# Kernel optimization log

Hardware: AMD Instinct MI355X
Metric: run time of the kernel (lower is better)

Reference implementation:

```python
import jax, jax.numpy as jnp
import numpy as np

N, E, B, M = 50000, 100000, 50, 50
NPG = N // B            # atoms per graph
DIN, H1, H2, DE, AAF, G = 32, 32, 64, 16, 95, 128
K, T = 3, 6             # ARMA num_stacks, num_layers
F1, F2, F3 = 64, 32, 16
EA = 2 * (M - 1)        # amino-acid edges per graph


def setup_inputs() -> dict:
    key = jax.random.key(0)
    ks = jax.random.split(key, 24)
    s = 0.05
    def w(k, shape):
        return jax.random.normal(k, shape, jnp.float32) * s
    return {
        "x": jax.random.normal(ks[0], (N, DIN), jnp.float32),
        "edge_attr": jax.random.normal(ks[1], (E, DE), jnp.float32),
        "aa_features": jax.random.normal(ks[2], (B, M, AAF), jnp.float32),
        "edge_index": jax.random.randint(ks[3], (2, E), 0, N),
        "monomer_labels": jax.random.randint(ks[4], (B, NPG), 0, M),
        "amino_edge_index": jax.random.randint(ks[5], (2, EA), 0, M),
        "W_e1": w(ks[6], (DE, DIN * H1)), "b_e1": jnp.zeros((DIN * H1,), jnp.float32),
        "root1": w(ks[7], (DIN, H1)), "bias1": jnp.zeros((H1,), jnp.float32),
        "W_e2": w(ks[8], (DE, H1 * H2)), "b_e2": jnp.zeros((H1 * H2,), jnp.float32),
        "root2": w(ks[9], (H1, H2)), "bias2": jnp.zeros((H2,), jnp.float32),
        "Wa_atom": w(ks[10], (H2, 1)), "ba_atom": jnp.zeros((1,), jnp.float32),
        "arma_init_w": w(ks[11], (K, H2 + AAF, G)),
        "arma_w": w(ks[12], (T - 1, K, G, G)),
        "arma_root_w": w(ks[13], (T, K, H2 + AAF, G)),
        "arma_bias": jnp.zeros((T, K, G), jnp.float32),
        "Wa_aa": w(ks[14], (G, 1)), "ba_aa": jnp.zeros((1,), jnp.float32),
        "W1": w(ks[15], (G, F1)), "b1": jnp.zeros((F1,), jnp.float32),
        "W2": w(ks[16], (F1, F2)), "b2": jnp.zeros((F2,), jnp.float32),
        "W3": w(ks[17], (F2, F3)), "b3": jnp.zeros((F3,), jnp.float32),
        "W4": w(ks[18], (F3, 1)), "b4": jnp.zeros((1,), jnp.float32),
    }


def _nnconv(h, src, dst, edge_attr, Wm, bm, root, bias, fin, fout):
    # NNConv (aggr='add'): edge MLP -> per-edge weight matrix, gather-matmul-scatter
    w_e = (edge_attr @ Wm + bm).reshape(-1, fin, fout)            # [E, fin, fout]
    msg = jnp.einsum('ef,efo->eo', h[src], w_e)                   # [E, fout]
    agg = jax.ops.segment_sum(msg, dst, num_segments=h.shape[0])  # scatter-add to targets
    return agg + h @ root + bias


def _forward(x, edge_attr, aa_features, W_e1, b_e1, root1, bias1, W_e2, b_e2, root2, bias2,
             Wa_atom, ba_atom, arma_init_w, arma_w, arma_root_w, arma_bias, Wa_aa, ba_aa,
             W1, b1, W2, b2, W3, b3, W4, b4, edge_index, monomer_labels, amino_edge_index):
    src, dst = edge_index[0], edge_index[1]
    h = jax.nn.relu(_nnconv(x, src, dst, edge_attr, W_e1, b_e1, root1, bias1, DIN, H1))
    h = jax.nn.relu(_nnconv(h, src, dst, edge_attr, W_e2, b_e2, root2, bias2, H1, H2))

    # per-graph attention readout over atoms -> amino-acid embeddings (scatter by monomer label)
    xg = h.reshape(B, NPG, H2)
    attn = jax.nn.softmax(xg @ Wa_atom + ba_atom, axis=1)         # softmax over atoms in graph
    wx = xg * attn
    aa = jax.vmap(lambda wxi, lbl: jax.ops.segment_sum(wxi, lbl, num_segments=M))(wx, monomer_labels)
    h_aa = jnp.concatenate([aa, aa_features], axis=-1)            # [B, M, H2+95]

    # ARMAConv: gcn_norm without self-loops on amino-acid graph (shared across graphs)
    asrc, adst = amino_edge_index[0], amino_edge_index[1]
    deg = jax.ops.segment_sum(jnp.ones((EA,), x.dtype), adst, num_segments=M)
    dinv = jnp.where(deg > 0, 1.0 / jnp.sqrt(jnp.maximum(deg, 1.0)), 0.0)
    norm = dinv[asrc] * dinv[adst]                                # [EA]

    def arma(x0):  # x0: [M, H2+95]
        out = jnp.einsum('mf,kfo->kmo', x0, arma_init_w)          # [K, M, G]
        for t in range(T):
            if t > 0:
                out = jnp.einsum('kmo,kop->kmp', out, arma_w[t - 1])
            msg = out[:, asrc] * norm[None, :, None]              # [K, EA, G]
            prop = jax.vmap(lambda m: jax.ops.segment_sum(m, adst, num_segments=M))(msg)
            rootc = jnp.einsum('mf,kfo->kmo', x0, arma_root_w[t])
            out = jax.nn.relu(prop + rootc + arma_bias[t][:, None, :])
        return out.mean(axis=0)                                   # mean over stacks -> [M, G]

    g = jax.vmap(arma)(h_aa)                                      # [B, M, G]

    # attention readout over amino acids
    attn2 = jax.nn.softmax(g @ Wa_aa + ba_aa, axis=1)
    p = jnp.sum(g * attn2, axis=1)                                # [B, G]

    p = jax.nn.relu(p @ W1 + b1)
    p = jax.nn.relu(p @ W2 + b2)
    p = jax.nn.relu(p @ W3 + b3)
    p = p @ W4 + b4
    return p.reshape(-1)                                          # [B]


def reference(x, edge_attr, aa_features, edge_index, monomer_labels, amino_edge_index,
              W_e1, b_e1, root1, bias1, W_e2, b_e2, root2, bias2, Wa_atom, ba_atom,
              arma_init_w, arma_w, arma_root_w, arma_bias, Wa_aa, ba_aa,
              W1, b1, W2, b2, W3, b3, W4, b4):
    return _forward(x, edge_attr, aa_features, W_e1, b_e1, root1, bias1, W_e2, b_e2, root2, bias2,
                    Wa_atom, ba_atom, arma_init_w, arma_w, arma_root_w, arma_bias, Wa_aa, ba_aa,
                    W1, b1, W2, b2, W3, b3, W4, b4, edge_index, monomer_labels, amino_edge_index)
```

## Files before the change

### kernel.cpp

```cpp
#include <hip/hip_runtime.h>
#include <math.h>

#define N_ATOMS 50000
#define E_EDGES 100000
#define B_G     50
#define M_M     50
#define NPG     1000
#define DIN     32
#define H1C     32
#define H2C     64
#define DEC     16
#define AAF     95
#define G_DIM   128
#define K_ST    3
#define T_L     6
#define EA_E    98
#define XDIM    159
#define NS      21
#define MPAD    64
#define GP      132
#define GPS     136
#define KP2     168
#define KW      544
#define SLC     10
#define APB     100
#define NSB     ((N_ATOMS + 255) / 256)

#define OFF_WE2 (H1C * KW)
#define OFF_WT  (OFF_WE2 + H2C * KW)
#define OFF_AW  (OFF_WT + NS * XDIM * G_DIM)
#define OFF_DEG (OFF_AW + (T_L - 1) * K_ST * G_DIM * G_DIM)
#define PREP_TOTAL (OFF_DEG + E_EDGES)

typedef __attribute__((ext_vector_type(8))) short bf16x8;
typedef __attribute__((ext_vector_type(4))) float f32x4;
typedef __attribute__((ext_vector_type(4))) unsigned int u32x4;

__device__ __forceinline__ short f2bf(float f) {
    unsigned int u = __float_as_uint(f);
    unsigned int r = (u + 0x7FFFu + ((u >> 16) & 1u)) >> 16;
    return (short)r;
}
__device__ __forceinline__ float bf2f(short b) {
    return __uint_as_float(((unsigned int)(unsigned short)b) << 16);
}
__device__ __forceinline__ unsigned int cvtpk_bf16(float lo, float hi) {
    unsigned int r;
    asm("v_cvt_pk_bf16_f32 %0, %1, %2" : "=v"(r) : "v"(lo), "v"(hi));
    return r;
}

__device__ __forceinline__ void f4fma(float4& d, float s, const float4& v) {
    d.x += s * v.x; d.y += s * v.y; d.z += s * v.z; d.w += s * v.w;
}
__device__ __forceinline__ void f4add(float4& d, const float4& v) {
    d.x += v.x; d.y += v.y; d.z += v.z; d.w += v.w;
}
__device__ __forceinline__ void f4relu(float4& d) {
    d.x = fmaxf(d.x, 0.f); d.y = fmaxf(d.y, 0.f);
    d.z = fmaxf(d.z, 0.f); d.w = fmaxf(d.w, 0.f);
}

__global__ __launch_bounds__(256) void prep_all(
    const float* __restrict__ We1, const float* __restrict__ be1, short* __restrict__ WB1,
    const float* __restrict__ We2, const float* __restrict__ be2, short* __restrict__ WB2,
    const float* __restrict__ init_w, const float* __restrict__ root_w, short* __restrict__ Wtb,
    const float* __restrict__ arma_w, short* __restrict__ Wab,
    const int* __restrict__ eidx, int* __restrict__ deg,
    const int* __restrict__ aei, int* __restrict__ aa_off,
    int* __restrict__ aa_src, float* __restrict__ aa_nrm)
{
    int tid = threadIdx.x;
    if (blockIdx.x == 0) {
        __shared__ int   sdeg[M_M];
        __shared__ int   scur[M_M];
        __shared__ float sdinv[M_M];
        __shared__ int   soff[M_M + 1];
        if (tid < M_M) { sdeg[tid] = 0; scur[tid] = 0; }
        __syncthreads();
        if (tid < EA_E) atomicAdd(&sdeg[aei[EA_E + tid]], 1);
        __syncthreads();
        if (tid < M_M) {
            float dv = (float)sdeg[tid];
            sdinv[tid] = (dv > 0.f) ? (1.f / sqrtf(fmaxf(dv, 1.f))) : 0.f;
        }
        __syncthreads();
        if (tid == 0) {
            soff[0] = 0;
            for (int m = 0; m < M_M; ++m) soff[m + 1] = soff[m] + sdeg[m];
        }
        __syncthreads();
        if (tid < EA_E) {
            int ss = aei[tid], dd = aei[EA_E + tid];
            int pos = atomicAdd(&scur[dd], 1);
            int idx = soff[dd] + pos;
            aa_src[idx] = ss;
            aa_nrm[idx] = sdinv[ss] * sdinv[dd];
        }
        if (tid < M_M + 1) aa_off[tid] = soff[tid];
        return;
    }
    int idx = (blockIdx.x - 1) * 256 + tid;
    if (idx < OFF_WE2) {
        int o = idx / KW, k = idx - o * KW;
        float v = (k < 512) ? We1[(size_t)k * H1C + o]
                            : be1[(size_t)(k - 512) * H1C + o];
        WB1[idx] = f2bf(v);
    } else if (idx < OFF_WT) {
        int rem = idx - OFF_WE2;
        int o = rem / KW, k = rem - o * KW;
        float v = (k < 512) ? We2[(size_t)k * H2C + o]
                            : be2[(size_t)(k - 512) * H2C + o];
        WB2[rem] = f2bf(v);
    } else if (idx < OFF_AW) {
        int rem = idx - OFF_WT;
        int s = rem / (XDIM * G_DIM);
        int r2 = rem - s * XDIM * G_DIM;
        int k = r2 / G_DIM, n = r2 - k * G_DIM;
        float v = (s < K_ST) ? init_w[rem]
                             : root_w[(size_t)(s - K_ST) * XDIM * G_DIM + r2];
        Wtb[(size_t)s * G_DIM * KP2 + n * KP2 + k] = f2bf(v);
    } else if (idx < OFF_DEG) {
        int rem = idx - OFF_AW;
        int slot = rem / (G_DIM * G_DIM);
        int r2 = rem - slot * G_DIM * G_DIM;
        int p = r2 / G_DIM, n = r2 - p * G_DIM;
        Wab[(size_t)slot * G_DIM * G_DIM + n * G_DIM + p] = f2bf(arma_w[rem]);
    } else if (idx < PREP_TOTAL) {
        int e = idx - OFF_DEG;
        atomicAdd(&deg[eidx[E_EDGES + e]], 1);
    }
}

__global__ __launch_bounds__(256) void scan_part(const int* __restrict__ deg,
                                                 int* __restrict__ bsum)
{
    __shared__ int tmp[256];
    int tid = threadIdx.x;
    int n = blockIdx.x * 256 + tid;
    tmp[tid] = (n < N_ATOMS) ? deg[n] : 0;
    __syncthreads();
    for (int off = 128; off > 0; off >>= 1) {
        if (tid < off) tmp[tid] += tmp[tid + off];
        __syncthreads();
    }
    if (tid == 0) bsum[blockIdx.x] = tmp[0];
}

__global__ __launch_bounds__(256) void scan_mid(const int* __restrict__ bsum,
                                                int* __restrict__ bpre)
{
    __shared__ int tmp[256];
    int tid = threadIdx.x;
    int v = (tid < NSB) ? bsum[tid] : 0;
    tmp[tid] = v;
    __syncthreads();
    for (int off = 1; off < 256; off <<= 1) {
        int t = tmp[tid];
        int add = (tid >= off) ? tmp[tid - off] : 0;
        __syncthreads();
        tmp[tid] = t + add;
        __syncthreads();
    }
    if (tid < NSB) bpre[tid] = tmp[tid] - v;
}

__global__ __launch_bounds__(256) void scan_out(int* __restrict__ deg_off,
                                                const int* __restrict__ bpre)
{
    __shared__ int tmp[256];
    int tid = threadIdx.x;
    int n = blockIdx.x * 256 + tid;
    int v = (n < N_ATOMS) ? deg_off[n] : 0;
    tmp[tid] = v;
    __syncthreads();
    for (int off = 1; off < 256; off <<= 1) {
        int t = tmp[tid];
        int add = (tid >= off) ? tmp[tid - off] : 0;
        __syncthreads();
        tmp[tid] = t + add;
        __syncthreads();
    }
    int incl = tmp[tid];
    int base = bpre[blockIdx.x];
    if (n < N_ATOMS) deg_off[n] = base + incl - v;
    if (n == N_ATOMS - 1) deg_off[N_ATOMS] = base + incl;
}

template<int FOUT, int NTT, int WGRP, int MTB, bool CIPOS>
__global__ __launch_bounds__(256) void edge_msg_v2(
    const float* __restrict__ h, const float* __restrict__ ea,
    const int* __restrict__ eidx, int* __restrict__ ipos,
    const int* __restrict__ off, int* __restrict__ cursor,
    const short* __restrict__ WB, float* __restrict__ msg)
{
    constexpr int KS = 17;
    __shared__ int iplds[MTB * 16];
    int tid  = threadIdx.x;
    int lane = tid & 63, wave = tid >> 6;
    int l16  = lane & 15, quad = lane >> 4;
    int nt   = wave % NTT, tg = wave / NTT;
    int ebase = blockIdx.x * (MTB * 16);

    if (CIPOS) {
        if (tid < MTB * 16) {
            int e = ebase + tid;
            if (e < E_EDGES) {
                int d = eidx[E_EDGES + e];
                int pos = atomicAdd(&cursor[d], 1);
                int p = off[d] + pos;
                iplds[tid] = p;
                ipos[e] = p;
            }
        }
    }

    bf16x8 Bfr[KS];
    {
        const short* wb = WB + (size_t)(nt * 16 + l16) * KW;
        #pragma unroll
        for (int ks = 0; ks < KS; ++ks)
            Bfr[ks] = *(const bf16x8*)(wb + ks * 32 + quad * 8);
    }
    if (CIPOS) __syncthreads();

    for (int t = tg; t < MTB; t += WGRP) {
        int e  = ebase + t * 16 + l16;
        int es = (e < E_EDGES) ? e : (E_EDGES - 1);
        int s  = eidx[es];
        float4 h0 = *(const float4*)(h + (size_t)s * 32 + quad * 8);
        float4 h1 = *(const float4*)(h + (size_t)s * 32 + quad * 8 + 4);
        float hf[8] = {h0.x, h0.y, h0.z, h0.w, h1.x, h1.y, h1.z, h1.w};
        float4 e0 = *(const float4*)(ea + (size_t)es * DEC);
        float4 e1 = *(const float4*)(ea + (size_t)es * DEC + 4);
        float4 e2 = *(const float4*)(ea + (size_t)es * DEC + 8);
        float4 e3 = *(const float4*)(ea + (size_t)es * DEC + 12);
        float eaf[16] = {e0.x, e0.y, e0.z, e0.w, e1.x, e1.y, e1.z, e1.w,
                         e2.x, e2.y, e2.z, e2.w, e3.x, e3.y, e3.z, e3.w};

        f32x4 acc = (f32x4){0.f, 0.f, 0.f, 0.f};
        #pragma unroll
        for (int ks = 0; ks < KS; ++ks) {
            u32x4 av;
            if (ks < DEC) {
                float fac = eaf[ks];
                #pragma unroll
                for (int j = 0; j < 4; ++j)
                    av[j] = cvtpk_bf16(fac * hf[2 * j], fac * hf[2 * j + 1]);
            } else {
                #pragma unroll
                for (int j = 0; j < 4; ++j)
                    av[j] = cvtpk_bf16(hf[2 * j], hf[2 * j + 1]);
            }
            bf16x8 a = __builtin_bit_cast(bf16x8, av);
            acc = __builtin_amdgcn_mfma_f32_16x16x32_bf16(a, Bfr[ks], acc, 0, 0, 0);
        }
        int erb = ebase + t * 16 + quad * 4;
        #pragma unroll
        for (int r = 0; r < 4; ++r) {
            int ee = erb + r;
            if (ee < E_EDGES) {
                int p = CIPOS ? iplds[t * 16 + quad * 4 + r] : ipos[ee];
                msg[(size_t)p * FOUT + nt * 16 + l16] = acc[r];
            }
        }
    }
}

template<int FIN, int FOUT, bool SCORE>
__global__ __launch_bounds__(256) void gather_update(
    const float* __restrict__ msg, const int* __restrict__ off,
    const float* __restrict__ hin,
    const float* __restrict__ root, const float* __restrict__ bias,
    float* __restrict__ hout,
    const float* __restrict__ wa, const float* __restrict__ ba,
    float* __restrict__ sc)
{
    constexpr int NPB = 256 / FOUT;
    __shared__ float rlds[FIN][FOUT];
    __shared__ float hlds[NPB][FIN];
    int tid = threadIdx.x;
    for (int i = tid; i < FIN * FOUT / 4; i += 256) {
        *(float4*)&rlds[0][i * 4] = *(const float4*)(root + i * 4);
    }
    int nb = blockIdx.x * NPB;
    for (int i = tid; i < NPB * FIN; i += 256) {
        int ln = i / FIN, f = i % FIN;
        int n = nb + ln;
        hlds[ln][f] = (n < N_ATOMS) ? hin[(size_t)n * FIN + f] : 0.f;
    }
    __syncthreads();

    int ln = tid / FOUT, o = tid % FOUT;
    int n = nb + ln;
    if (n >= N_ATOMS) return;
    float acc = bias[o];
    #pragma unroll 8
    for (int f = 0; f < FIN; ++f) acc += hlds[ln][f] * rlds[f][o];
    int j0 = off[n], j1 = off[n + 1];
    for (int j = j0; j < j1; ++j) {
        acc += msg[(size_t)j * FOUT + o];
    }
    float hv = fmaxf(acc, 0.f);
    hout[(size_t)n * FOUT + o] = hv;
    if constexpr (SCORE) {
        static_assert(FOUT == 64, "score fusion needs node==wave");
        float sv = hv * wa[o];
        #pragma unroll
        for (int d = 32; d > 0; d >>= 1) sv += __shfl_down(sv, d);
        if (o == 0) sc[n] = sv + ba[0];
    }
}

__global__ __launch_bounds__(256) void atom_scatter_sm(
    const float* __restrict__ h2, const float* __restrict__ sc,
    const int* __restrict__ labels, float* __restrict__ partial)
{
    __shared__ float aa4[4][M_M][H2C];
    __shared__ float red[256];
    int b = blockIdx.x / SLC, s = blockIdx.x % SLC;
    int tid = threadIdx.x;
    int wave = tid >> 6, lane = tid & 63;
    const float* sb = sc + (size_t)b * NPG;

    for (int i = tid; i < 4 * M_M * H2C; i += 256) ((float*)aa4)[i] = 0.f;

    float lmax = -1e30f;
    for (int n = tid; n < NPG; n += 256) lmax = fmaxf(lmax, sb[n]);
    red[tid] = lmax;
    __syncthreads();
    for (int off = 128; off > 0; off >>= 1) {
        if (tid < off) red[tid] = fmaxf(red[tid], red[tid + off]);
        __syncthreads();
    }
    float mx = red[0];
    __syncthreads();
    float lsum = 0.f;
    for (int n = tid; n < NPG; n += 256) lsum += expf(sb[n] - mx);
    red[tid] = lsum;
    __syncthreads();
    for (int off = 128; off > 0; off >>= 1) {
        if (tid < off) red[tid] += red[tid + off];
        __syncthreads();
    }
    float inv = 1.f / red[0];
    __syncthreads();

    int nbase = s * APB;
    const float* hb = h2 + (size_t)b * NPG * H2C;
    #pragma unroll 5
    for (int it = 0; it < APB / 4; ++it) {
        int n = nbase + it * 4 + wave;
        int lbl = labels[b * NPG + n];
        float w = expf(sb[n] - mx) * inv;
        float hv = hb[(size_t)n * H2C + lane];
        aa4[wave][lbl][lane] += hv * w;
    }
    __syncthreads();
    float* pb = partial + (size_t)(b * SLC + s) * M_M * H2C;
    for (int i = tid; i < M_M * H2C; i += 256) {
        float v = ((float*)aa4)[i] + ((float*)aa4)[M_M * H2C + i]
                + ((float*)aa4)[2 * M_M * H2C + i] + ((float*)aa4)[3 * M_M * H2C + i];
        pb[i] = v;
    }
}

__global__ __launch_bounds__(256) void x0_finalize(
    const float* __restrict__ partial, const float* __restrict__ aaf,
    short* __restrict__ x0b)
{
    int idx = blockIdx.x * 256 + threadIdx.x;
    if (idx >= B_G * MPAD * KP2) return;
    int b = idx / (MPAD * KP2);
    int rem = idx - b * (MPAD * KP2);
    int m = rem / KP2, k = rem - m * KP2;
    float v = 0.f;
    if (m < M_M) {
        if (k < H2C) {
            const float* pb = partial + (size_t)b * SLC * M_M * H2C + m * H2C + k;
            #pragma unroll
            for (int s = 0; s < SLC; ++s) v += pb[(size_t)s * (M_M * H2C)];
        } else if (k < XDIM) {
            v = aaf[((size_t)b * M_M + m) * AAF + (k - H2C)];
        }
    }
    x0b[idx] = f2bf(v);
}

__global__ __launch_bounds__(512) void arma_iter(
    const short* __restrict__ x0b, const short* __restrict__ Wtb,
    const short* __restrict__ Wab, const float* __restrict__ arma_bias,
    const int* __restrict__ aa_off, const int* __restrict__ aa_src,
    const float* __restrict__ aa_nrm, float* __restrict__ gfull)
{
    __shared__ float Abuf[MPAD][GP];
    __shared__ float Rall[3][MPAD][GP];
    __shared__ short Bb16[MPAD][GPS];
    __shared__ int   s_off[M_M + 1];
    __shared__ int   s_src[EA_E];
    __shared__ float s_nrm[EA_E];
    int b = blockIdx.x / K_ST, k = blockIdx.x % K_ST;
    int tid = threadIdx.x;
    int oi = tid & 15, mi = tid >> 4;
    int c0 = oi * 4, c1 = 64 + oi * 4;
    int lane = tid & 63, wave = tid >> 6;
    int l16 = lane & 15, quad = lane >> 4;
    int mt = wave >> 1, nh = wave & 1;

    if (tid < M_M + 1) s_off[tid] = aa_off[tid];
    if (tid < EA_E) { s_src[tid] = aa_src[tid]; s_nrm[tid] = aa_nrm[tid]; }
    for (int i = tid; i < MPAD * GPS / 2; i += 512) {
        ((int*)Bb16)[i] = 0;
    }

    bf16x8 Afr[5];
    {
        const short* xb = x0b + (size_t)b * MPAD * KP2 + (mt * 16 + l16) * KP2;
        #pragma unroll
        for (int ks = 0; ks < 5; ++ks)
            Afr[ks] = *(const bf16x8*)(xb + ks * 32 + quad * 8);
    }

    auto x0_gemm = [&](const short* __restrict__ W, float (*dst)[GP]) {
        f32x4 acc[4];
        #pragma unroll
        for (int nt = 0; nt < 4; ++nt) acc[nt] = (f32x4){0.f, 0.f, 0.f, 0.f};
        #pragma unroll
        for (int ks = 0; ks < 5; ++ks) {
            #pragma unroll
            for (int nt = 0; nt < 4; ++nt) {
                int n0 = (nh * 4 + nt) * 16 + l16;
                bf16x8 bf = *(const bf16x8*)(W + (size_t)n0 * KP2 + ks * 32 + quad * 8);
                acc[nt] = __builtin_amdgcn_mfma_f32_16x16x32_bf16(Afr[ks], bf, acc[nt], 0, 0, 0);
            }
        }
        #pragma unroll
        for (int nt = 0; nt < 4; ++nt) {
            #pragma unroll
            for (int r = 0; r < 4; ++r) {
                dst[mt * 16 + quad * 4 + r][(nh * 4 + nt) * 16 + l16] = acc[nt][r];
            }
        }
    };

    x0_gemm(Wtb + (size_t)k * G_DIM * KP2, Abuf);
    #pragma unroll
    for (int t = 0; t < 3; ++t)
        x0_gemm(Wtb + (size_t)(K_ST + t * K_ST + k) * G_DIM * KP2, Rall[t]);

    float* gb = gfull + ((size_t)(b * K_ST + k)) * M_M * G_DIM;
    __syncthreads();

    #pragma unroll
    for (int t = 0; t < T_L; ++t) {
        if (t > 0) {
            const short* aw = Wab + (size_t)((t - 1) * K_ST + k) * G_DIM * G_DIM;
            f32x4 acc[4];
            #pragma unroll
            for (int nt = 0; nt < 4; ++nt) acc[nt] = (f32x4){0.f, 0.f, 0.f, 0.f};
            #pragma unroll
            for (int ks = 0; ks < 4; ++ks) {
                bf16x8 a = *(const bf16x8*)&Bb16[mt * 16 + l16][ks * 32 + quad * 8];
                #pragma unroll
                for (int nt = 0; nt < 4; ++nt) {
                    int n0 = (nh * 4 + nt) * 16 + l16;
                    bf16x8 bf = *(const bf16x8*)(aw + n0 * G_DIM + ks * 32 + quad * 8);
                    acc[nt] = __builtin_amdgcn_mfma_f32_16x16x32_bf16(a, bf, acc[nt], 0, 0, 0);
                }
            }
            #pragma unroll
            for (int nt = 0; nt < 4; ++nt)
                #pragma unroll
                for (int r = 0; r < 4; ++r)
                    Abuf[mt * 16 + quad * 4 + r][(nh * 4 + nt) * 16 + l16] = acc[nt][r];
            if (t == 3) {
                #pragma unroll
                for (int tt = 3; tt < 6; ++tt)
                    x0_gemm(Wtb + (size_t)(K_ST + tt * K_ST + k) * G_DIM * KP2,
                            Rall[tt - 3]);
            }
            __syncthreads();
        }
        const float (*Rb)[GP] = Rall[t % 3];
        const float* bb = arma_bias + ((size_t)t * K_ST + k) * G_DIM;
        float4 bias0 = *(const float4*)(bb + c0);
        float4 bias1 = *(const float4*)(bb + c1);
        #pragma unroll
        for (int r = 0; r < 2; ++r) {
            int m = mi * 2 + r;
            if (m < M_M) {
                float4 v0 = bias0, v1 = bias1;
                f4add(v0, *(const float4*)&Rb[m][c0]);
                f4add(v1, *(const float4*)&Rb[m][c1]);
                int j0 = s_off[m], j1 = s_off[m + 1];
                for (int j = j0; j < j1; ++j) {
                    float nv = s_nrm[j];
                    const float* ap = &Abuf[s_src[j]][0];
                    f4fma(v0, nv, *(const float4*)(ap + c0));
                    f4fma(v1, nv, *(const float4*)(ap + c1));
                }
                f4relu(v0);
                f4relu(v1);
                unsigned int p0 = cvtpk_bf16(v0.x, v0.y);
                unsigned int p1 = cvtpk_bf16(v0.z, v0.w);
                unsigned int p2 = cvtpk_bf16(v1.x, v1.y);
                unsigned int p3 = cvtpk_bf16(v1.z, v1.w);
                *(uint2*)&Bb16[m][c0] = make_uint2(p0, p1);
                *(uint2*)&Bb16[m][c1] = make_uint2(p2, p3);
                if (t == T_L - 1) {
                    *(float4*)(gb + m * G_DIM + c0) = v0;
                    *(float4*)(gb + m * G_DIM + c1) = v1;
                }
            }
        }
        __syncthreads();
    }
}

__global__ __launch_bounds__(128) void aa_readout_mlp(
    const float* __restrict__ gfull, const float* __restrict__ wa,
    const float* __restrict__ ba,
    const float* __restrict__ W1, const float* __restrict__ b1,
    const float* __restrict__ W2, const float* __restrict__ b2,
    const float* __restrict__ W3, const float* __restrict__ b3,
    const float* __restrict__ W4, const float* __restrict__ b4,
    float* __restrict__ out)
{
    __shared__ float g[M_M][G_DIM + 1];
    __shared__ float s2[M_M];
    __shared__ float p[G_DIM];
    __shared__ float r1[64], r2[32], r3[16];
    int b = blockIdx.x, tid = threadIdx.x;
    const float* g0 = gfull + (size_t)b * K_ST * M_M * G_DIM;
    for (int i = tid; i < M_M * G_DIM; i += 128) {
        int m = i >> 7, o = i & 127;
        g[m][o] = (g0[i] + g0[M_M*G_DIM + i] + g0[2*M_M*G_DIM + i]) * (1.f/3.f);
    }
    __syncthreads();
    if (tid < M_M) {
        float sv = ba[0];
        for (int o = 0; o < G_DIM; ++o) sv += g[tid][o] * wa[o];
        s2[tid] = sv;
    }
    __syncthreads();
    if (tid == 0) {
        float mx = -1e30f;
        for (int m = 0; m < M_M; ++m) mx = fmaxf(mx, s2[m]);
        float den = 0.f;
        for (int m = 0; m < M_M; ++m) den += expf(s2[m] - mx);
        float inv = 1.f / den;
        for (int m = 0; m < M_M; ++m) s2[m] = expf(s2[m] - mx) * inv;
    }
    __syncthreads();
    {
        float pv = 0.f;
        for (int m = 0; m < M_M; ++m) pv += g[m][tid] * s2[m];
        p[tid] = pv;
    }
    __syncthreads();
    if (tid < 64) {
        float v = b1[tid];
        for (int i = 0; i < 128; ++i) v += p[i] * W1[i * 64 + tid];
        r1[tid] = fmaxf(v, 0.f);
    }
    __syncthreads();
    if (tid < 32) {
        float v = b2[tid];
        for (int i = 0; i < 64; ++i) v += r1[i] * W2[i * 32 + tid];
        r2[tid] = fmaxf(v, 0.f);
    }
    __syncthreads();
    if (tid < 16) {
        float v = b3[tid];
        for (int i = 0; i < 32; ++i) v += r2[i] * W3[i * 16 + tid];
        r3[tid] = fmaxf(v, 0.f);
    }
    __syncthreads();
    if (tid == 0) {
        float v = b4[0];
        for (int i = 0; i < 16; ++i) v += r3[i] * W4[i];
        out[b] = v;
    }
}

extern "C" void kernel_launch(void* const* d_in, const int* in_sizes, int n_in,
                              void* d_out, int out_size, void* d_ws, size_t ws_size,
                              hipStream_t stream)
{
    (void)in_sizes; (void)n_in; (void)out_size; (void)ws_size;
    const float* x            = (const float*)d_in[0];
    const float* edge_attr    = (const float*)d_in[1];
    const float* aa_features  = (const float*)d_in[2];
    const int*   edge_index   = (const int*)  d_in[3];
    const int*   mono_labels  = (const int*)  d_in[4];
    const int*   amino_ei     = (const int*)  d_in[5];
    const float* W_e1 = (const float*)d_in[6];
    const float* b_e1 = (const float*)d_in[7];
    const float* root1= (const float*)d_in[8];
    const float* bias1= (const float*)d_in[9];
    const float* W_e2 = (const float*)d_in[10];
    const float* b_e2 = (const float*)d_in[11];
    const float* root2= (const float*)d_in[12];
    const float* bias2= (const float*)d_in[13];
    const float* Wa_atom = (const float*)d_in[14];
    const float* ba_atom = (const float*)d_in[15];
    const float* arma_init_w = (const float*)d_in[16];
    const float* arma_w      = (const float*)d_in[17];
    const float* arma_root_w = (const float*)d_in[18];
    const float* arma_bias   = (const float*)d_in[19];
    const float* Wa_aa = (const float*)d_in[20];
    const float* ba_aa = (const float*)d_in[21];
    const float* W1 = (const float*)d_in[22];
    const float* b1 = (const float*)d_in[23];
    const float* W2 = (const float*)d_in[24];
    const float* b2 = (const float*)d_in[25];
    const float* W3 = (const float*)d_in[26];
    const float* b3 = (const float*)d_in[27];
    const float* W4 = (const float*)d_in[28];
    const float* b4 = (const float*)d_in[29];

    float* ws = (float*)d_ws;
    float* h1    = ws;
    float* h2    = h1   + (size_t)N_ATOMS * H1C;
    float* h_aa  = h2   + (size_t)N_ATOMS * H2C;
    float* sc    = h_aa + (size_t)B_G * M_M * XDIM;
    int*   aa_off = (int*)(sc + (size_t)B_G * NPG);
    int*   aa_src = aa_off + (M_M + 1);
    float* aa_nrm = (float*)(aa_src + EA_E);
    int*   deg_off = (int*)(aa_nrm + EA_E);
    int*   cursor  = deg_off + (N_ATOMS + 1);
    int*   ipos    = cursor + N_ATOMS;
    int*   bsum    = ipos + E_EDGES;
    int*   bpre    = bsum + 256;
    float* RC    = (float*)(bpre + 256);
    float* gfull = RC + (size_t)B_G * NS * M_M * G_DIM;
    short* Wtb   = (short*)((((uintptr_t)(gfull + (size_t)B_G * K_ST * M_M * G_DIM)) + 15)
                            & ~(uintptr_t)15);
    short* x0b   = Wtb + (size_t)NS * G_DIM * KP2;
    short* Wab   = x0b + (size_t)B_G * MPAD * KP2;
    short* WB1   = Wab + (size_t)(T_L - 1) * K_ST * G_DIM * G_DIM;
    short* WB2   = WB1 + (size_t)H1C * KW;
    float* msg   = RC;
    float* partial = RC;
    (void)h_aa;

    (void)hipMemsetAsync(deg_off, 0, (2 * N_ATOMS + 1) * sizeof(int), stream);

    prep_all<<<1 + (PREP_TOTAL + 255) / 256, 256, 0, stream>>>(
        W_e1, b_e1, WB1, W_e2, b_e2, WB2,
        arma_init_w, arma_root_w, Wtb, arma_w, Wab,
        edge_index, deg_off, amino_ei, aa_off, aa_src, aa_nrm);

    scan_part<<<NSB, 256, 0, stream>>>(deg_off, bsum);
    scan_mid<<<1, 256, 0, stream>>>(bsum, bpre);
    scan_out<<<NSB, 256, 0, stream>>>(deg_off, bpre);

    edge_msg_v2<H1C, 2, 2, 8, true><<<(E_EDGES + 127) / 128, 256, 0, stream>>>(
        x, edge_attr, edge_index, ipos, deg_off, cursor, WB1, msg);
    gather_update<DIN, H1C, false><<<(N_ATOMS + 7) / 8, 256, 0, stream>>>(
        msg, deg_off, x, root1, bias1, h1, nullptr, nullptr, nullptr);
    edge_msg_v2<H2C, 4, 1, 8, false><<<(E_EDGES + 127) / 128, 256, 0, stream>>>(
        h1, edge_attr, edge_index, ipos, nullptr, nullptr, WB2, msg);
    gather_update<H1C, H2C, true><<<(N_ATOMS + 3) / 4, 256, 0, stream>>>(
        msg, deg_off, h1, root2, bias2, h2, Wa_atom, ba_atom, sc);

    atom_scatter_sm<<<B_G * SLC, 256, 0, stream>>>(h2, sc, mono_labels, partial);
    x0_finalize<<<(B_G * MPAD * KP2 + 255) / 256, 256, 0, stream>>>(
        partial, aa_features, x0b);

    arma_iter<<<B_G * K_ST, 512, 0, stream>>>(x0b, Wtb, Wab, arma_bias,
                                              aa_off, aa_src, aa_nrm, gfull);
    aa_readout_mlp<<<B_G, 128, 0, stream>>>(gfull, Wa_aa, ba_aa, W1, b1, W2, b2, W3, b3, W4, b4,
                                            (float*)d_out);
}
```

Baseline: 302.6 us.

## Halve arma_iter block size and reuse weight fragments across two M tiles per wave

The ARMA kernel now runs with 256 threads instead of 512, so each wave computes two 16-row M tiles. Weight B-fragments for the x0 projection and the per-layer recurrent GEMM are loaded into registers once and reused for both tiles, which halves global weight loads per block. The propagation loop now covers four rows per thread instead of two. In exchange there are fewer waves to hide latency and register use per thread rises; launch_bounds(256,1) lets the compiler spend those registers.

```diff
diff --git a/kernel.cpp b/kernel.cpp
--- a/kernel.cpp
+++ b/kernel.cpp
@@ -387,7 +387,7 @@
     x0b[idx] = f2bf(v);
 }
 
-__global__ __launch_bounds__(512) void arma_iter(
+__global__ __launch_bounds__(256, 1) void arma_iter(
     const short* __restrict__ x0b, const short* __restrict__ Wtb,
     const short* __restrict__ Wab, const float* __restrict__ arma_bias,
     const int* __restrict__ aa_off, const int* __restrict__ aa_src,
@@ -405,41 +405,49 @@
     int c0 = oi * 4, c1 = 64 + oi * 4;
     int lane = tid & 63, wave = tid >> 6;
     int l16 = lane & 15, quad = lane >> 4;
-    int mt = wave >> 1, nh = wave & 1;
+    int w2 = wave >> 1, nh = wave & 1;
 
     if (tid < M_M + 1) s_off[tid] = aa_off[tid];
     if (tid < EA_E) { s_src[tid] = aa_src[tid]; s_nrm[tid] = aa_nrm[tid]; }
-    for (int i = tid; i < MPAD * GPS / 2; i += 512) {
+    for (int i = tid; i < MPAD * GPS / 2; i += 256) {
         ((int*)Bb16)[i] = 0;
     }
 
-    bf16x8 Afr[5];
-    {
+    bf16x8 Afr[2][5];
+    #pragma unroll
+    for (int h = 0; h < 2; ++h) {
+        int mt = w2 + 2 * h;
         const short* xb = x0b + (size_t)b * MPAD * KP2 + (mt * 16 + l16) * KP2;
         #pragma unroll
         for (int ks = 0; ks < 5; ++ks)
-            Afr[ks] = *(const bf16x8*)(xb + ks * 32 + quad * 8);
+            Afr[h][ks] = *(const bf16x8*)(xb + ks * 32 + quad * 8);
     }
 
     auto x0_gemm = [&](const short* __restrict__ W, float (*dst)[GP]) {
-        f32x4 acc[4];
-        #pragma unroll
-        for (int nt = 0; nt < 4; ++nt) acc[nt] = (f32x4){0.f, 0.f, 0.f, 0.f};
-        #pragma unroll
-        for (int ks = 0; ks < 5; ++ks) {
+        bf16x8 Bfr[5][4];
+        #pragma unroll
+        for (int ks = 0; ks < 5; ++ks)
             #pragma unroll
-            for (int nt = 0; nt < 4; ++nt) {
-                int n0 = (nh * 4 + nt) * 16 + l16;
-                bf16x8 bf = *(const bf16x8*)(W + (size_t)n0 * KP2 + ks * 32 + quad * 8);
-                acc[nt] = __builtin_amdgcn_mfma_f32_16x16x32_bf16(Afr[ks], bf, acc[nt], 0, 0, 0);
-            }
-        }
-        #pragma unroll
-        for (int nt = 0; nt < 4; ++nt) {
+            for (int nt = 0; nt < 4; ++nt)
+                Bfr[ks][nt] = *(const bf16x8*)(W +
+                    (size_t)((nh * 4 + nt) * 16 + l16) * KP2 + ks * 32 + quad * 8);
+        #pragma unroll
+        for (int h = 0; h < 2; ++h) {
+            int mt = w2 + 2 * h;
+            f32x4 acc[4];
             #pragma unroll
-            for (int r = 0; r < 4; ++r) {
-                dst[mt * 16 + quad * 4 + r][(nh * 4 + nt) * 16 + l16] = acc[nt][r];
-            }
+            for (int nt = 0; nt < 4; ++nt) acc[nt] = (f32x4){0.f, 0.f, 0.f, 0.f};
+            #pragma unroll
+            for (int ks = 0; ks < 5; ++ks)
+                #pragma unroll
+                for (int nt = 0; nt < 4; ++nt)
+                    acc[nt] = __builtin_amdgcn_mfma_f32_16x16x32_bf16(
+                        Afr[h][ks], Bfr[ks][nt], acc[nt], 0, 0, 0);
+            #pragma unroll
+            for (int nt = 0; nt < 4; ++nt)
+                #pragma unroll
+                for (int r = 0; r < 4; ++r)
+                    dst[mt * 16 + quad * 4 + r][(nh * 4 + nt) * 16 + l16] = acc[nt][r];
         }
     };
 
@@ -455,24 +463,33 @@
     for (int t = 0; t < T_L; ++t) {
         if (t > 0) {
             const short* aw = Wab + (size_t)((t - 1) * K_ST + k) * G_DIM * G_DIM;
-            f32x4 acc[4];
+            bf16x8 Wfr[4][4];
             #pragma unroll
-            for (int nt = 0; nt < 4; ++nt) acc[nt] = (f32x4){0.f, 0.f, 0.f, 0.f};
+            for (int ks = 0; ks < 4; ++ks)
+                #pragma unroll
+                for (int nt = 0; nt < 4; ++nt)
+                    Wfr[ks][nt] = *(const bf16x8*)(aw +
+                        (size_t)((nh * 4 + nt) * 16 + l16) * G_DIM + ks * 32 + quad * 8);
             #pragma unroll
-            for (int ks = 0; ks < 4; ++ks) {
-                bf16x8 a = *(const bf16x8*)&Bb16[mt * 16 + l16][ks * 32 + quad * 8];
-                #pragma unroll
-                for (int nt = 0; nt < 4; ++nt) {
-                    int n0 = (nh * 4 + nt) * 16 + l16;
-                    bf16x8 bf = *(const bf16x8*)(aw + n0 * G_DIM + ks * 32 + quad * 8);
-                    acc[nt] = __builtin_amdgcn_mfma_f32_16x16x32_bf16(a, bf, acc[nt], 0, 0, 0);
+            for (int h = 0; h < 2; ++h) {
+                int mt = w2 + 2 * h;
+                f32x4 acc[4];
+                #pragma unroll
+                for (int nt = 0; nt < 4; ++nt) acc[nt] = (f32x4){0.f, 0.f, 0.f, 0.f};
+                #pragma unroll
+                for (int ks = 0; ks < 4; ++ks) {
+                    bf16x8 a = *(const bf16x8*)&Bb16[mt * 16 + l16][ks * 32 + quad * 8];
+                    #pragma unroll
+                    for (int nt = 0; nt < 4; ++nt)
+                        acc[nt] = __builtin_amdgcn_mfma_f32_16x16x32_bf16(
+                            a, Wfr[ks][nt], acc[nt], 0, 0, 0);
                 }
+                #pragma unroll
+                for (int nt = 0; nt < 4; ++nt)
+                    #pragma unroll
+                    for (int r = 0; r < 4; ++r)
+                        Abuf[mt * 16 + quad * 4 + r][(nh * 4 + nt) * 16 + l16] = acc[nt][r];
             }
-            #pragma unroll
-            for (int nt = 0; nt < 4; ++nt)
-                #pragma unroll
-                for (int r = 0; r < 4; ++r)
-                    Abuf[mt * 16 + quad * 4 + r][(nh * 4 + nt) * 16 + l16] = acc[nt][r];
             if (t == 3) {
                 #pragma unroll
                 for (int tt = 3; tt < 6; ++tt)
@@ -486,8 +503,8 @@
         float4 bias0 = *(const float4*)(bb + c0);
         float4 bias1 = *(const float4*)(bb + c1);
         #pragma unroll
-        for (int r = 0; r < 2; ++r) {
-            int m = mi * 2 + r;
+        for (int r = 0; r < 4; ++r) {
+            int m = mi * 4 + r;
             if (m < M_M) {
                 float4 v0 = bias0, v1 = bias1;
                 f4add(v0, *(const float4*)&Rb[m][c0]);
@@ -668,7 +685,7 @@
     x0_finalize<<<(B_G * MPAD * KP2 + 255) / 256, 256, 0, stream>>>(
         partial, aa_features, x0b);
 
-    arma_iter<<<B_G * K_ST, 512, 0, stream>>>(x0b, Wtb, Wab, arma_bias,
+    arma_iter<<<B_G * K_ST, 256, 0, stream>>>(x0b, Wtb, Wab, arma_bias,
                                               aa_off, aa_src, aa_nrm, gfull);
     aa_readout_mlp<<<B_G, 128, 0, stream>>>(gfull, Wa_aa, ba_aa, W1, b1, W2, b2, W3, b3, W4, b4,
                                             (float*)d_out);
```

New measurement: 295.5 us. 2.3% less time.
